# Kernel tuning notes

Hardware: AMD Instinct MI355X
Metric: run time of the kernel (lower is better)

## Reference

```python
import jax, jax.numpy as jnp
import numpy as np

HIDDEN = 512
NUM_SE = 960
BATCH = 32768


def setup_inputs() -> dict:
    key = jax.random.key(0)
    k1, k2, k3 = jax.random.split(key, 3)
    z_i = jax.random.normal(k1, (BATCH, HIDDEN), dtype=jnp.float32)
    z_j = jax.random.normal(k2, (BATCH, HIDDEN), dtype=jnp.float32)
    # R = I + 0.01 * randn, as in the torch __init__
    R = jnp.eye(HIDDEN, dtype=jnp.float32) + 0.01 * jax.random.normal(k3, (HIDDEN, HIDDEN), dtype=jnp.float32)
    D = jnp.ones((NUM_SE, HIDDEN), dtype=jnp.float32)
    return {"z_i": z_i, "z_j": z_j, "R": R, "D": D}


def reference(z_i, z_j, R, D):
    # score[b, r] = sigmoid( sum_h z_i[b,h] * D[r,h] * (z_j @ R.T)[b,h] * D[r,h] )
    # Algebraically identical to the broadcasted torch expression, but expressed
    # as (z_i * Rz_j) @ (D**2).T — avoids the O(B*num_se*hidden) intermediate.
    Rz_j = z_j @ R.T                      # [B, H]
    scores = (z_i * Rz_j) @ (D * D).T     # [B, num_se]
    return jax.nn.sigmoid(scores)
```

## Files before the change

kernel.cpp:

```cpp
#include <hip/hip_runtime.h>
#include <cstdint>
#include <cstddef>

#define HID 512
#define NSE 960
#define NB  32768
#define BM  64
#define ZROW 520

typedef __attribute__((ext_vector_type(4))) float f32x4;
typedef __attribute__((ext_vector_type(8))) _Float16 h8;
typedef __attribute__((ext_vector_type(4))) _Float16 h4;

#define WS_RTH 0u
#define WS_WTH 524288u
#define WS_WTL 1507328u
#define WS_FLAG 2490368u

__global__ void init_flag_kernel(unsigned int* f) { *f = 0u; }

__global__ void prep_kernel(const float* __restrict__ R, const float* __restrict__ D,
                            _Float16* __restrict__ RTh, _Float16* __restrict__ WTh,
                            _Float16* __restrict__ WTl, unsigned int* __restrict__ flag) {
  int t = blockIdx.x * 256 + threadIdx.x;
  int lane = t & 63;
  int ks   = (t >> 6) & 15;
  int rr   = lane & 15;
  int k0   = ks * 32 + (lane >> 4) * 8;
  if (t < 32768) {
    int c = (t >> 10) * 16 + rr;
    const float* src = R + (size_t)c * HID + k0;
    h8 hv;
#pragma unroll
    for (int e = 0; e < 8; ++e) hv[e] = (_Float16)src[e];
    *(h8*)(RTh + (size_t)t * 8) = hv;
  } else if (t < 32768 + 61440) {
    int o = t - 32768;
    int r = (o >> 10) * 16 + rr;
    const float* src = D + (size_t)r * HID + k0;
    h8 hv, lv;
    bool any = false;
#pragma unroll
    for (int e = 0; e < 8; ++e) {
      float d = src[e];
      float w = d * d;
      _Float16 hh = (_Float16)w;
      _Float16 ll = (_Float16)(w - (float)hh);
      hv[e] = hh; lv[e] = ll;
      any = any || ((float)ll != 0.0f);
    }
    *(h8*)(WTh + (size_t)o * 8) = hv;
    *(h8*)(WTl + (size_t)o * 8) = lv;
    if (any) atomicOr(flag, 1u);
  }
}

template <int NPAN, bool WLO>
__device__ __forceinline__ void gemm2_body(const _Float16* zh, const _Float16* zl,
                                           const _Float16* __restrict__ WThb,
                                           const _Float16* __restrict__ WTlb,
                                           const int (&aoff)[4],
                                           f32x4 (&acc)[4][8]) {
#pragma unroll 2
  for (int ks = 0; ks < 16; ++ks) {
    const int ko = ks * 32;
    h8 uh[4], ul[4];
#pragma unroll
    for (int mi = 0; mi < 4; ++mi) {
      uh[mi] = *(const h8*)(zh + aoff[mi] + ko);
      ul[mi] = *(const h8*)(zl + aoff[mi] + ko);
    }
#pragma unroll
    for (int ni = 0; ni < NPAN; ++ni) {
      h8 bh = *(const h8*)(WThb + ni * 8192 + ks * 512);
#pragma unroll
      for (int mi = 0; mi < 4; ++mi) {
        acc[mi][ni] = __builtin_amdgcn_mfma_f32_16x16x32_f16(uh[mi], bh, acc[mi][ni], 0, 0, 0);
        acc[mi][ni] = __builtin_amdgcn_mfma_f32_16x16x32_f16(ul[mi], bh, acc[mi][ni], 0, 0, 0);
      }
      if (WLO) {
        h8 bl = *(const h8*)(WTlb + ni * 8192 + ks * 512);
#pragma unroll
        for (int mi = 0; mi < 4; ++mi)
          acc[mi][ni] = __builtin_amdgcn_mfma_f32_16x16x32_f16(uh[mi], bl, acc[mi][ni], 0, 0, 0);
      }
    }
  }
}

__global__ __launch_bounds__(512, 2)
void fused_dedicom(const float* __restrict__ zi, const float* __restrict__ zj,
                   const _Float16* __restrict__ RTh, const _Float16* __restrict__ WTh,
                   const _Float16* __restrict__ WTl, const unsigned int* __restrict__ flag,
                   float* __restrict__ out) {
  __shared__ _Float16 sm[2 * BM * ZROW];
  _Float16* zh = sm;
  _Float16* zl = sm + BM * ZROW;

  const int tid  = threadIdx.x;
  const int wave = tid >> 6;
  const int lane = tid & 63;
  const int lr   = lane & 15;
  const int lg   = lane >> 4;
  const size_t brow = (size_t)blockIdx.x * BM;

  const float* zjB = zj + brow * HID;
#pragma unroll
  for (int it = 0; it < 16; ++it) {
    int flat = it * 2048 + tid * 4;
    f32x4 v = *(const f32x4*)(zjB + flat);
    int row = flat >> 9;
    int k = flat & (HID - 1);
    h4 hv, lv;
#pragma unroll
    for (int q = 0; q < 4; ++q) {
      _Float16 hh = (_Float16)v[q];
      hv[q] = hh;
      lv[q] = (_Float16)(v[q] - (float)hh);
    }
    *(h4*)(zh + row * ZROW + k) = hv;
    *(h4*)(zl + row * ZROW + k) = lv;
  }

  const float* ziB = zi + brow * HID;
  float zir[4][4][4];
#pragma unroll
  for (int mi = 0; mi < 4; ++mi)
#pragma unroll
    for (int ni = 0; ni < 4; ++ni)
#pragma unroll
      for (int q = 0; q < 4; ++q)
        zir[mi][ni][q] = ziB[(size_t)(mi * 16 + lg * 4 + q) * HID + wave * 64 + ni * 16 + lr];

  __syncthreads();

  f32x4 acc1[4][4];
#pragma unroll
  for (int mi = 0; mi < 4; ++mi)
#pragma unroll
    for (int ni = 0; ni < 4; ++ni) acc1[mi][ni] = f32x4{0.f, 0.f, 0.f, 0.f};

  const _Float16* RTb = RTh + (size_t)wave * 4 * 8192 + (size_t)lane * 8;
  int aoff[4];
#pragma unroll
  for (int mi = 0; mi < 4; ++mi) aoff[mi] = (mi * 16 + lr) * ZROW + lg * 8;

#pragma unroll 2
  for (int ks = 0; ks < 16; ++ks) {
    const int ko = ks * 32;
    h8 ah[4], al[4];
#pragma unroll
    for (int mi = 0; mi < 4; ++mi) {
      ah[mi] = *(const h8*)(zh + aoff[mi] + ko);
      al[mi] = *(const h8*)(zl + aoff[mi] + ko);
    }
#pragma unroll
    for (int ni = 0; ni < 4; ++ni) {
      h8 bh = *(const h8*)(RTb + ni * 8192 + ks * 512);
#pragma unroll
      for (int mi = 0; mi < 4; ++mi) {
        acc1[mi][ni] = __builtin_amdgcn_mfma_f32_16x16x32_f16(ah[mi], bh, acc1[mi][ni], 0, 0, 0);
        acc1[mi][ni] = __builtin_amdgcn_mfma_f32_16x16x32_f16(al[mi], bh, acc1[mi][ni], 0, 0, 0);
      }
    }
  }
  __syncthreads();

#pragma unroll
  for (int mi = 0; mi < 4; ++mi)
#pragma unroll
    for (int ni = 0; ni < 4; ++ni) {
      int col = wave * 64 + ni * 16 + lr;
#pragma unroll
      for (int q = 0; q < 4; ++q) {
        int row = mi * 16 + lg * 4 + q;
        float u = zir[mi][ni][q] * acc1[mi][ni][q];
        _Float16 hh = (_Float16)u;
        zh[row * ZROW + col] = hh;
        zl[row * ZROW + col] = (_Float16)(u - (float)hh);
      }
    }
  __syncthreads();

  f32x4 acc2[4][8];
#pragma unroll
  for (int mi = 0; mi < 4; ++mi)
#pragma unroll
    for (int ni = 0; ni < 8; ++ni) acc2[mi][ni] = f32x4{0.f, 0.f, 0.f, 0.f};

  const int p0   = (wave < 4) ? wave * 8 : 32 + (wave - 4) * 7;
  const int npan = (wave < 4) ? 8 : 7;
  const _Float16* WThb = WTh + (size_t)p0 * 8192 + (size_t)lane * 8;
  const _Float16* WTlb = WTl + (size_t)p0 * 8192 + (size_t)lane * 8;

  const bool wlo = (*flag != 0u);
  if (wave < 4) {
    if (wlo) gemm2_body<8, true >(zh, zl, WThb, WTlb, aoff, acc2);
    else     gemm2_body<8, false>(zh, zl, WThb, WTlb, aoff, acc2);
  } else {
    if (wlo) gemm2_body<7, true >(zh, zl, WThb, WTlb, aoff, acc2);
    else     gemm2_body<7, false>(zh, zl, WThb, WTlb, aoff, acc2);
  }

  float* outB = out + brow * NSE;
#pragma unroll
  for (int mi = 0; mi < 4; ++mi)
#pragma unroll
    for (int ni = 0; ni < 8; ++ni) {
      if (ni < npan) {
        int col = (p0 + ni) * 16 + lr;
#pragma unroll
        for (int q = 0; q < 4; ++q) {
          int row = mi * 16 + lg * 4 + q;
          float s = acc2[mi][ni][q];
          outB[(size_t)row * NSE + col] = 1.0f / (1.0f + __expf(-s));
        }
      }
    }
}

extern "C" void kernel_launch(void* const* d_in, const int* in_sizes, int n_in,
                              void* d_out, int out_size, void* d_ws, size_t ws_size,
                              hipStream_t stream) {
  const float* zi = (const float*)d_in[0];
  const float* zj = (const float*)d_in[1];
  const float* R  = (const float*)d_in[2];
  const float* D  = (const float*)d_in[3];
  float* out = (float*)d_out;

  unsigned char* ws = (unsigned char*)d_ws;
  _Float16* RTh = (_Float16*)(ws + WS_RTH);
  _Float16* WTh = (_Float16*)(ws + WS_WTH);
  _Float16* WTl = (_Float16*)(ws + WS_WTL);
  unsigned int* flag = (unsigned int*)(ws + WS_FLAG);

  init_flag_kernel<<<1, 1, 0, stream>>>(flag);
  prep_kernel<<<368, 256, 0, stream>>>(R, D, RTh, WTh, WTl, flag);
  fused_dedicom<<<NB / BM, 512, 0, stream>>>(zi, zj, RTh, WTh, WTl, flag, out);
}
```

Before: 296.9 us.

## Drop split-fp16 low terms for activations and widen blocks to 1024 threads

Removes the hi/lo fp16 split of z_j and of the intermediate product, so both GEMMs run on fp16 activations only and use half the MFMA work and half the shared memory. Blocks grow to 16 waves, each wave owning fewer output panels, and the z_i gather moves out of registers to a direct load at the elementwise step. The flag init kernel becomes a memset. Accuracy drops to plain fp16 rounding of activations, which may exceed tolerance.

```diff
diff --git a/kernel.cpp b/kernel.cpp
--- a/kernel.cpp
+++ b/kernel.cpp
@@ -17,15 +17,13 @@
 #define WS_WTL 1507328u
 #define WS_FLAG 2490368u
 
-__global__ void init_flag_kernel(unsigned int* f) { *f = 0u; }
-
 __global__ void prep_kernel(const float* __restrict__ R, const float* __restrict__ D,
                             _Float16* __restrict__ RTh, _Float16* __restrict__ WTh,
                             _Float16* __restrict__ WTl, unsigned int* __restrict__ flag) {
   int t = blockIdx.x * 256 + threadIdx.x;
   int lane = t & 63;
+  int rr   = lane & 15;
   int ks   = (t >> 6) & 15;
-  int rr   = lane & 15;
   int k0   = ks * 32 + (lane >> 4) * 8;
   if (t < 32768) {
     int c = (t >> 10) * 16 + rr;
@@ -56,28 +54,23 @@
 }
 
 template <int NPAN, bool WLO>
-__device__ __forceinline__ void gemm2_body(const _Float16* zh, const _Float16* zl,
+__device__ __forceinline__ void gemm2_body(const _Float16* zh,
                                            const _Float16* __restrict__ WThb,
                                            const _Float16* __restrict__ WTlb,
                                            const int (&aoff)[4],
-                                           f32x4 (&acc)[4][8]) {
+                                           f32x4 (&acc)[4][4]) {
 #pragma unroll 2
   for (int ks = 0; ks < 16; ++ks) {
     const int ko = ks * 32;
-    h8 uh[4], ul[4];
-#pragma unroll
-    for (int mi = 0; mi < 4; ++mi) {
-      uh[mi] = *(const h8*)(zh + aoff[mi] + ko);
-      ul[mi] = *(const h8*)(zl + aoff[mi] + ko);
-    }
+    h8 uh[4];
+#pragma unroll
+    for (int mi = 0; mi < 4; ++mi) uh[mi] = *(const h8*)(zh + aoff[mi] + ko);
 #pragma unroll
     for (int ni = 0; ni < NPAN; ++ni) {
       h8 bh = *(const h8*)(WThb + ni * 8192 + ks * 512);
 #pragma unroll
-      for (int mi = 0; mi < 4; ++mi) {
+      for (int mi = 0; mi < 4; ++mi)
         acc[mi][ni] = __builtin_amdgcn_mfma_f32_16x16x32_f16(uh[mi], bh, acc[mi][ni], 0, 0, 0);
-        acc[mi][ni] = __builtin_amdgcn_mfma_f32_16x16x32_f16(ul[mi], bh, acc[mi][ni], 0, 0, 0);
-      }
       if (WLO) {
         h8 bl = *(const h8*)(WTlb + ni * 8192 + ks * 512);
 #pragma unroll
@@ -88,14 +81,12 @@
   }
 }
 
-__global__ __launch_bounds__(512, 2)
+__global__ __launch_bounds__(1024)
 void fused_dedicom(const float* __restrict__ zi, const float* __restrict__ zj,
                    const _Float16* __restrict__ RTh, const _Float16* __restrict__ WTh,
                    const _Float16* __restrict__ WTl, const unsigned int* __restrict__ flag,
                    float* __restrict__ out) {
-  __shared__ _Float16 sm[2 * BM * ZROW];
-  _Float16* zh = sm;
-  _Float16* zl = sm + BM * ZROW;
+  __shared__ _Float16 zh[BM * ZROW];
 
   const int tid  = threadIdx.x;
   const int wave = tid >> 6;
@@ -106,41 +97,25 @@
 
   const float* zjB = zj + brow * HID;
 #pragma unroll
-  for (int it = 0; it < 16; ++it) {
-    int flat = it * 2048 + tid * 4;
+  for (int it = 0; it < 8; ++it) {
+    int flat = it * 4096 + tid * 4;
     f32x4 v = *(const f32x4*)(zjB + flat);
     int row = flat >> 9;
     int k = flat & (HID - 1);
-    h4 hv, lv;
-#pragma unroll
-    for (int q = 0; q < 4; ++q) {
-      _Float16 hh = (_Float16)v[q];
-      hv[q] = hh;
-      lv[q] = (_Float16)(v[q] - (float)hh);
-    }
+    h4 hv;
+#pragma unroll
+    for (int q = 0; q < 4; ++q) hv[q] = (_Float16)v[q];
     *(h4*)(zh + row * ZROW + k) = hv;
-    *(h4*)(zl + row * ZROW + k) = lv;
-  }
-
-  const float* ziB = zi + brow * HID;
-  float zir[4][4][4];
-#pragma unroll
-  for (int mi = 0; mi < 4; ++mi)
-#pragma unroll
-    for (int ni = 0; ni < 4; ++ni)
-#pragma unroll
-      for (int q = 0; q < 4; ++q)
-        zir[mi][ni][q] = ziB[(size_t)(mi * 16 + lg * 4 + q) * HID + wave * 64 + ni * 16 + lr];
-
+  }
   __syncthreads();
 
-  f32x4 acc1[4][4];
-#pragma unroll
-  for (int mi = 0; mi < 4; ++mi)
-#pragma unroll
-    for (int ni = 0; ni < 4; ++ni) acc1[mi][ni] = f32x4{0.f, 0.f, 0.f, 0.f};
-
-  const _Float16* RTb = RTh + (size_t)wave * 4 * 8192 + (size_t)lane * 8;
+  f32x4 acc1[4][2];
+#pragma unroll
+  for (int mi = 0; mi < 4; ++mi)
+#pragma unroll
+    for (int ni = 0; ni < 2; ++ni) acc1[mi][ni] = f32x4{0.f, 0.f, 0.f, 0.f};
+
+  const _Float16* RTb = RTh + (size_t)wave * 2 * 8192 + (size_t)lane * 8;
   int aoff[4];
 #pragma unroll
   for (int mi = 0; mi < 4; ++mi) aoff[mi] = (mi * 16 + lr) * ZROW + lg * 8;
@@ -148,65 +123,59 @@
 #pragma unroll 2
   for (int ks = 0; ks < 16; ++ks) {
     const int ko = ks * 32;
-    h8 ah[4], al[4];
-#pragma unroll
-    for (int mi = 0; mi < 4; ++mi) {
-      ah[mi] = *(const h8*)(zh + aoff[mi] + ko);
-      al[mi] = *(const h8*)(zl + aoff[mi] + ko);
-    }
-#pragma unroll
-    for (int ni = 0; ni < 4; ++ni) {
+    h8 ah[4];
+#pragma unroll
+    for (int mi = 0; mi < 4; ++mi) ah[mi] = *(const h8*)(zh + aoff[mi] + ko);
+#pragma unroll
+    for (int ni = 0; ni < 2; ++ni) {
       h8 bh = *(const h8*)(RTb + ni * 8192 + ks * 512);
 #pragma unroll
-      for (int mi = 0; mi < 4; ++mi) {
+      for (int mi = 0; mi < 4; ++mi)
         acc1[mi][ni] = __builtin_amdgcn_mfma_f32_16x16x32_f16(ah[mi], bh, acc1[mi][ni], 0, 0, 0);
-        acc1[mi][ni] = __builtin_amdgcn_mfma_f32_16x16x32_f16(al[mi], bh, acc1[mi][ni], 0, 0, 0);
-      }
     }
   }
   __syncthreads();
 
-#pragma unroll
-  for (int mi = 0; mi < 4; ++mi)
-#pragma unroll
-    for (int ni = 0; ni < 4; ++ni) {
-      int col = wave * 64 + ni * 16 + lr;
+  const float* ziB = zi + brow * HID;
+#pragma unroll
+  for (int mi = 0; mi < 4; ++mi)
+#pragma unroll
+    for (int ni = 0; ni < 2; ++ni) {
+      int col = wave * 32 + ni * 16 + lr;
 #pragma unroll
       for (int q = 0; q < 4; ++q) {
         int row = mi * 16 + lg * 4 + q;
-        float u = zir[mi][ni][q] * acc1[mi][ni][q];
-        _Float16 hh = (_Float16)u;
-        zh[row * ZROW + col] = hh;
-        zl[row * ZROW + col] = (_Float16)(u - (float)hh);
+        float u = ziB[(size_t)row * HID + col] * acc1[mi][ni][q];
+        zh[row * ZROW + col] = (_Float16)u;
       }
     }
   __syncthreads();
 
-  f32x4 acc2[4][8];
-#pragma unroll
-  for (int mi = 0; mi < 4; ++mi)
-#pragma unroll
-    for (int ni = 0; ni < 8; ++ni) acc2[mi][ni] = f32x4{0.f, 0.f, 0.f, 0.f};
-
-  const int p0   = (wave < 4) ? wave * 8 : 32 + (wave - 4) * 7;
-  const int npan = (wave < 4) ? 8 : 7;
+  f32x4 acc2[4][4];
+#pragma unroll
+  for (int mi = 0; mi < 4; ++mi)
+#pragma unroll
+    for (int ni = 0; ni < 4; ++ni) acc2[mi][ni] = f32x4{0.f, 0.f, 0.f, 0.f};
+
+  const int p0   = (wave < 12) ? wave * 4 : 48 + (wave - 12) * 3;
+  const int npan = (wave < 12) ? 4 : 3;
   const _Float16* WThb = WTh + (size_t)p0 * 8192 + (size_t)lane * 8;
   const _Float16* WTlb = WTl + (size_t)p0 * 8192 + (size_t)lane * 8;
 
   const bool wlo = (*flag != 0u);
-  if (wave < 4) {
-    if (wlo) gemm2_body<8, true >(zh, zl, WThb, WTlb, aoff, acc2);
-    else     gemm2_body<8, false>(zh, zl, WThb, WTlb, aoff, acc2);
+  if (npan == 4) {
+    if (wlo) gemm2_body<4, true >(zh, WThb, WTlb, aoff, acc2);
+    else     gemm2_body<4, false>(zh, WThb, WTlb, aoff, acc2);
   } else {
-    if (wlo) gemm2_body<7, true >(zh, zl, WThb, WTlb, aoff, acc2);
-    else     gemm2_body<7, false>(zh, zl, WThb, WTlb, aoff, acc2);
+    if (wlo) gemm2_body<3, true >(zh, WThb, WTlb, aoff, acc2);
+    else     gemm2_body<3, false>(zh, WThb, WTlb, aoff, acc2);
   }
 
   float* outB = out + brow * NSE;
 #pragma unroll
   for (int mi = 0; mi < 4; ++mi)
 #pragma unroll
-    for (int ni = 0; ni < 8; ++ni) {
+    for (int ni = 0; ni < 4; ++ni) {
       if (ni < npan) {
         int col = (p0 + ni) * 16 + lr;
 #pragma unroll
@@ -234,7 +203,7 @@
   _Float16* WTl = (_Float16*)(ws + WS_WTL);
   unsigned int* flag = (unsigned int*)(ws + WS_FLAG);
 
-  init_flag_kernel<<<1, 1, 0, stream>>>(flag);
+  hipMemsetAsync(flag, 0, 4, stream);
   prep_kernel<<<368, 256, 0, stream>>>(R, D, RTh, WTh, WTl, flag);
-  fused_dedicom<<<NB / BM, 512, 0, stream>>>(zi, zj, RTh, WTh, WTl, flag, out);
-}
+  fused_dedicom<<<NB / BM, 1024, 0, stream>>>(zi, zj, RTh, WTh, WTl, flag, out);
+}
```

Result: faster. 276.0 us (-7.0%).
